# Kernel tuning notes

Measured on AMD Instinct MI355X. Metric: run time of the kernel, lower is better.

## Reference

```python
import jax, jax.numpy as jnp
import numpy as np

N = 100_000   # nodes
E = 600_000   # edges per layer (avg degree ~6, ogbn-arxiv-like)
IN, H, C = 128, 256, 40


def _sage_layer(x, src, dst, w_self, w_neigh, b):
    """DGL SAGEConv with mean aggregator: fc_self(x) + fc_neigh(mean_nbr) + b."""
    n = x.shape[0]
    msg = x[src]                                               # [E, d] gather
    agg = jax.ops.segment_sum(msg, dst, num_segments=n)        # [N, d]
    deg = jax.ops.segment_sum(jnp.ones((src.shape[0],), x.dtype), dst,
                              num_segments=n)                  # [N]
    h_neigh = agg / jnp.maximum(deg, 1.0)[:, None]             # mean; 0 if isolated
    return x @ w_self.T + h_neigh @ w_neigh.T + b


def setup_inputs() -> dict:
    key = jax.random.key(0)
    ks = jax.random.split(key, 11)
    s = 0.02
    return {
        "x": jax.random.normal(ks[0], (N, IN), jnp.float32),
        "src1": jax.random.randint(ks[1], (E,), 0, N, jnp.int32),
        "dst1": jax.random.randint(ks[2], (E,), 0, N, jnp.int32),
        "src2": jax.random.randint(ks[3], (E,), 0, N, jnp.int32),
        "dst2": jax.random.randint(ks[4], (E,), 0, N, jnp.int32),
        "w_self1": s * jax.random.normal(ks[5], (H, IN), jnp.float32),
        "w_neigh1": s * jax.random.normal(ks[6], (H, IN), jnp.float32),
        "b1": jnp.zeros((H,), jnp.float32),
        "w_self2": s * jax.random.normal(ks[7], (C, H), jnp.float32),
        "w_neigh2": s * jax.random.normal(ks[8], (C, H), jnp.float32),
        "b2": jnp.zeros((C,), jnp.float32),
    }


def reference(x, src1, dst1, src2, dst2, w_self1, w_neigh1, b1,
              w_self2, w_neigh2, b2):
    h = jax.nn.relu(_sage_layer(x, src1, dst1, w_self1, w_neigh1, b1))
    return _sage_layer(h, src2, dst2, w_self2, w_neigh2, b2)
```

## Files before the change

### kernel.cpp

```cpp
#include <hip/hip_runtime.h>
#include <hip/hip_bf16.h>
#include <cstdint>
#include <cstddef>


#define D_IN 128
#define D_H  256
#define D_C  40

#define NBLK     128
#define NBKT_MAX 392
#define BKT_CAP  2560

typedef __bf16 bf16_t;
typedef __attribute__((ext_vector_type(8))) __bf16 bf16x8;
typedef __attribute__((ext_vector_type(4))) __bf16 bf16x4;
typedef __attribute__((ext_vector_type(4))) float  f32x4;

static constexpr size_t NMAX = 100000;
static constexpr size_t EMAX = 600000;
static constexpr size_t NSC_MAX = (size_t)NBKT_MAX * NBLK;
static constexpr size_t alignup(size_t v) { return (v + 255) & ~size_t(255); }

static constexpr size_t HG1_OFF  = 0;
static constexpr size_t HG2_OFF  = alignup(HG1_OFF + NSC_MAX * 4);
static constexpr size_t BS1_OFF  = alignup(HG2_OFF + NSC_MAX * 4);
static constexpr size_t BS2_OFF  = alignup(BS1_OFF + 512 * 4);
static constexpr size_t RP1_OFF  = alignup(BS2_OFF + 512 * 4);
static constexpr size_t RP2_OFF  = alignup(RP1_OFF + (NMAX + 1) * 4);
static constexpr size_t BKT1_OFF = alignup(RP2_OFF + (NMAX + 1) * 4);
static constexpr size_t BKT2_OFF = alignup(BKT1_OFF + EMAX * 4);
static constexpr size_t XCAT_OFF = alignup(BKT2_OFF + EMAX * 4);
static constexpr size_t P_OFF    = alignup(XCAT_OFF + (NMAX + 128) * 256 * 2);
static constexpr size_t W1F_OFF  = alignup(P_OFF + NMAX * 40 * 2);
static constexpr size_t W2F_OFF  = alignup(W1F_OFF + 32 * 256 * 8 * 2);
static constexpr size_t WS_NEEDED = W2F_OFF + 32 * 80 * 8 * 2;

__global__ __launch_bounds__(256) void k_prep(
    const float* __restrict__ x, bf16_t* __restrict__ xcat,
    const float* __restrict__ ws1, const float* __restrict__ wn1,
    const float* __restrict__ ws2, const float* __restrict__ wn2,
    bf16_t* __restrict__ w1f, bf16_t* __restrict__ w2f,
    const int* __restrict__ dst1, const int* __restrict__ dst2,
    int* __restrict__ hg1, int* __restrict__ hg2,
    int N, int E, int chunk, int nbkt, int nconvx) {
  __shared__ int h[NBKT_MAX];
  int bid = blockIdx.x;

  if (bid < nconvx) {
    int t = bid * 256 + threadIdx.x;
    if (t < N * 16) {
      int row = t >> 4, j = t & 15;
      const float* sp = x + (size_t)row * 128 + j * 8;
      float4 v0 = ((const float4*)sp)[0];
      float4 v1 = ((const float4*)sp)[1];
      bf16x8 o;
      o[0] = (bf16_t)v0.x; o[1] = (bf16_t)v0.y; o[2] = (bf16_t)v0.z; o[3] = (bf16_t)v0.w;
      o[4] = (bf16_t)v1.x; o[5] = (bf16_t)v1.y; o[6] = (bf16_t)v1.z; o[7] = (bf16_t)v1.w;
      *(bf16x8*)(xcat + (size_t)row * 256 + j * 8) = o;
    }
    return;
  }
  bid -= nconvx;

  if (bid < 32) {
    int t = bid * 256 + threadIdx.x;
    {
      int ks4g = t >> 8, col = t & 255;
      int k0 = (ks4g >> 2) * 32 + (ks4g & 3) * 8;
      bf16x8 o;
#pragma unroll
      for (int i = 0; i < 8; ++i) {
        int k = k0 + i;
        float v = (k < 128) ? ws1[col * 128 + k] : wn1[col * 128 + (k - 128)];
        o[i] = (bf16_t)v;
      }
      *(bf16x8*)(w1f + (size_t)t * 8) = o;
    }
    if (t < 32 * 80) {
      int ks4g = t / 80, col = t - ks4g * 80;
      int k0 = (ks4g >> 2) * 32 + (ks4g & 3) * 8;
      bf16x8 o;
#pragma unroll
      for (int i = 0; i < 8; ++i) {
        int k = k0 + i;
        float v = (col < 40) ? ws2[col * 256 + k] : wn2[(col - 40) * 256 + k];
        o[i] = (bf16_t)v;
      }
      *(bf16x8*)(w2f + (size_t)t * 8) = o;
    }
    return;
  }
  bid -= 32;
  {
    const int* dst = (bid >> 7) ? dst2 : dst1;
    int*       hg  = (bid >> 7) ? hg2 : hg1;
    int        cb  = bid & 127;
    for (int i = threadIdx.x; i < nbkt; i += 256) h[i] = 0;
    __syncthreads();
    int beg = cb * chunk, end = min(E, beg + chunk);
    for (int e = beg + threadIdx.x; e < end; e += 256)
      atomicAdd(&h[dst[e] >> 8], 1);
    __syncthreads();
    for (int b = threadIdx.x; b < nbkt; b += 256)
      hg[b * NBLK + cb] = h[b];
  }
}

__global__ void k_scan_block(int* __restrict__ a1, int* __restrict__ a2,
                             int* __restrict__ b1s, int* __restrict__ b2s, int n) {
  int* a    = blockIdx.y ? a2 : a1;
  int* bsum = blockIdx.y ? b2s : b1s;
  __shared__ int lds[256];
  int t = threadIdx.x, i = blockIdx.x * 256 + t;
  int v = (i < n) ? a[i] : 0;
  lds[t] = v;
  __syncthreads();
  for (int off = 1; off < 256; off <<= 1) {
    int add = (t >= off) ? lds[t - off] : 0;
    __syncthreads();
    lds[t] += add;
    __syncthreads();
  }
  if (i < n) a[i] = lds[t] - v;
  if (t == 255) bsum[blockIdx.x] = lds[255];
}

__global__ void k_scan_addsums(int* __restrict__ a1, int* __restrict__ a2,
                               const int* __restrict__ b1s, const int* __restrict__ b2s,
                               int n, int nb) {
  int* a          = blockIdx.y ? a2 : a1;
  const int* bsum = blockIdx.y ? b2s : b1s;
  __shared__ int lds[256];
  int t = threadIdx.x;
  int v = (t < nb) ? bsum[t] : 0;
  lds[t] = v;
  __syncthreads();
  for (int off = 1; off < 256; off <<= 1) {
    int add = (t >= off) ? lds[t - off] : 0;
    __syncthreads();
    lds[t] += add;
    __syncthreads();
  }
  __shared__ int excl[256];
  excl[t] = lds[t] - v;
  __syncthreads();
  int i = blockIdx.x * 256 + t;
  if (i < n) a[i] += excl[i >> 8];
}

__global__ void k_scat(const int* __restrict__ src1, const int* __restrict__ dst1,
                       const int* __restrict__ src2, const int* __restrict__ dst2,
                       const int* __restrict__ off1, const int* __restrict__ off2,
                       unsigned* __restrict__ bkt1, unsigned* __restrict__ bkt2,
                       int E, int chunk, int nbkt) {
  const int* src = blockIdx.y ? src2 : src1;
  const int* dst = blockIdx.y ? dst2 : dst1;
  const int* off = blockIdx.y ? off2 : off1;
  unsigned*  bkt = blockIdx.y ? bkt2 : bkt1;
  __shared__ int cur[NBKT_MAX];
  for (int i = threadIdx.x; i < nbkt; i += 256)
    cur[i] = off[i * NBLK + blockIdx.x];
  __syncthreads();
  int beg = blockIdx.x * chunk, end = min(E, beg + chunk);
  for (int e = beg + threadIdx.x; e < end; e += 256) {
    int d = dst[e];
    int slot = atomicAdd(&cur[d >> 8], 1);
    bkt[slot] = (unsigned)src[e] | ((unsigned)(d & 255) << 24);
  }
}

__global__ __launch_bounds__(256) void k_bcsr(
    const int* __restrict__ off1, const int* __restrict__ off2,
    const unsigned* bkt1, const unsigned* bkt2,
    int* csr1, int* csr2,
    int* __restrict__ rp1, int* __restrict__ rp2, int E, int N, int nbkt) {
  const int* off      = blockIdx.y ? off2 : off1;
  const unsigned* bkt = blockIdx.y ? bkt2 : bkt1;
  int* csr            = blockIdx.y ? csr2 : csr1;
  int* rowptr         = blockIdx.y ? rp2 : rp1;

  const int b = blockIdx.x, t = threadIdx.x;
  const int base = off[b * NBLK];
  const int endp = (b == nbkt - 1) ? E : off[(b + 1) * NBLK];
  const int cnt  = endp - base;

  __shared__ int hist[256];
  __shared__ int sc[256];
  __shared__ int cur[256];
  __shared__ int stage[BKT_CAP];

  hist[t] = 0;
  __syncthreads();
  for (int i = t; i < cnt; i += 256)
    atomicAdd(&hist[bkt[base + i] >> 24], 1);
  __syncthreads();

  int v = hist[t];
  sc[t] = v;
  __syncthreads();
  for (int off_ = 1; off_ < 256; off_ <<= 1) {
    int add = (t >= off_) ? sc[t - off_] : 0;
    __syncthreads();
    sc[t] += add;
    __syncthreads();
  }
  int excl = sc[t] - v;

  int node = b * 256 + t;
  if (node < N) rowptr[node] = base + excl;
  if (b == nbkt - 1 && t == 0) rowptr[N] = E;
  cur[t] = excl;
  __syncthreads();

  for (int i = t; i < cnt; i += 256) {
    unsigned u = bkt[base + i];
    int slot = atomicAdd(&cur[u >> 24], 1);
    if (slot < BKT_CAP) stage[slot] = (int)(u & 0xFFFFFFu);
  }
  __syncthreads();
  for (int i = t; i < cnt; i += 256)
    csr[base + i] = stage[i];
}

__global__ void k_agg1(bf16_t* __restrict__ xcat, const int* __restrict__ rowptr,
                       const int* __restrict__ csr, int N) {
  int t = blockIdx.x * 256 + threadIdx.x;
  int node = t >> 4, l = t & 15;
  if (node >= N) return;
  int beg = rowptr[node], end = rowptr[node + 1];
  float acc[8] = {0.f, 0.f, 0.f, 0.f, 0.f, 0.f, 0.f, 0.f};
  int e = beg;
  for (; e + 4 <= end; e += 4) {
    int s0 = csr[e], s1 = csr[e + 1], s2 = csr[e + 2], s3 = csr[e + 3];
    bf16x8 v0 = *(const bf16x8*)(xcat + (size_t)s0 * 256 + l * 8);
    bf16x8 v1 = *(const bf16x8*)(xcat + (size_t)s1 * 256 + l * 8);
    bf16x8 v2 = *(const bf16x8*)(xcat + (size_t)s2 * 256 + l * 8);
    bf16x8 v3 = *(const bf16x8*)(xcat + (size_t)s3 * 256 + l * 8);
#pragma unroll
    for (int i = 0; i < 8; ++i)
      acc[i] += (float)v0[i] + (float)v1[i] + (float)v2[i] + (float)v3[i];
  }
  for (; e < end; ++e) {
    int s = csr[e];
    bf16x8 v = *(const bf16x8*)(xcat + (size_t)s * 256 + l * 8);
#pragma unroll
    for (int i = 0; i < 8; ++i) acc[i] += (float)v[i];
  }
  float rd = (end > beg) ? 1.0f / (float)(end - beg) : 0.0f;
  bf16x8 o;
#pragma unroll
  for (int i = 0; i < 8; ++i) o[i] = (bf16_t)(acc[i] * rd);
  *(bf16x8*)(xcat + (size_t)node * 256 + 128 + l * 8) = o;
}

__global__ __launch_bounds__(256, 2) void k_fused(
    const bf16_t* __restrict__ xcat, const bf16_t* __restrict__ w1f,
    const float* __restrict__ b1, const bf16_t* __restrict__ w2f,
    const float* __restrict__ b2v, float* __restrict__ out,
    bf16_t* __restrict__ p, int N) {
  __shared__ __align__(16) char lds[65536];
  const int tid  = (int)threadIdx.x;
  const int wv   = tid >> 6;
  const int lane = tid & 63;
  const int lr   = lane & 15;
  const int lg   = lane >> 4;
  const int c0   = wv * 64;
  const int m0   = (int)blockIdx.x * 128;

  {
    const char* tb = (const char*)(xcat + (size_t)m0 * 256);
#pragma unroll
    for (int i = 0; i < 16; ++i) {
      int L   = i * 4096 + tid * 16;
      int row = L >> 9;
      int c   = L & 511;
      int so  = (row << 9) | (c ^ ((row & 7) << 4));
      __builtin_amdgcn_global_load_lds(
          (const __attribute__((address_space(1))) void*)(tb + so),
          (__attribute__((address_space(3))) void*)(lds + L), 16, 0, 0);
    }
  }
  __syncthreads();

  f32x4 acc[4][8] = {};
#pragma unroll
  for (int ks = 0; ks < 8; ++ks) {
    bf16x8 wf[4];
#pragma unroll
    for (int wb = 0; wb < 4; ++wb)
      wf[wb] = *(const bf16x8*)(w1f + ((size_t)(ks * 4 + lg) * 256 +
                                       (c0 + wb * 16 + lr)) * 8);
    bf16x8 ax[8];
#pragma unroll
    for (int rb = 0; rb < 8; ++rb) {
      int lrow = rb * 16 + lr;
      ax[rb] = *(const bf16x8*)(lds + lrow * 512 +
                                ((ks * 64 + lg * 16) ^ ((lrow & 7) << 4)));
    }
#pragma unroll
    for (int wb = 0; wb < 4; ++wb)
#pragma unroll
      for (int rb = 0; rb < 8; ++rb)
        acc[wb][rb] = __builtin_amdgcn_mfma_f32_16x16x32_bf16(
            wf[wb], ax[rb], acc[wb][rb], 0, 0, 0);
  }

  __syncthreads();

#pragma unroll
  for (int wb = 0; wb < 4; ++wb) {
    float4 b4 = *(const float4*)(b1 + c0 + wb * 16 + lg * 4);
#pragma unroll
    for (int rb = 0; rb < 8; ++rb) {
      int xrow = rb * 16 + lr;
      bf16x4 o;
      o[0] = (bf16_t)fmaxf(acc[wb][rb][0] + b4.x, 0.f);
      o[1] = (bf16_t)fmaxf(acc[wb][rb][1] + b4.y, 0.f);
      o[2] = (bf16_t)fmaxf(acc[wb][rb][2] + b4.z, 0.f);
      o[3] = (bf16_t)fmaxf(acc[wb][rb][3] + b4.w, 0.f);
      *(bf16x4*)(lds + xrow * 512 +
                 ((c0 * 2 + wb * 32 + lg * 8) ^ ((xrow & 7) << 4))) = o;
    }
  }
  __syncthreads();

  f32x4 acc2[2][5] = {};
#pragma unroll
  for (int ks = 0; ks < 8; ++ks) {
    bf16x8 hf[2];
#pragma unroll
    for (int m = 0; m < 2; ++m) {
      int arow = wv * 32 + m * 16 + lr;
      hf[m] = *(const bf16x8*)(lds + arow * 512 +
                               ((ks * 64 + lg * 16) ^ ((arow & 7) << 4)));
    }
#pragma unroll
    for (int wb = 0; wb < 5; ++wb) {
      bf16x8 w2 = *(const bf16x8*)(w2f + ((size_t)(ks * 4 + lg) * 80 +
                                          (wb * 16 + lr)) * 8);
#pragma unroll
      for (int m = 0; m < 2; ++m)
        acc2[m][wb] = __builtin_amdgcn_mfma_f32_16x16x32_bf16(
            w2, hf[m], acc2[m][wb], 0, 0, 0);
    }
  }

#pragma unroll
  for (int m = 0; m < 2; ++m) {
    const int r = m0 + wv * 32 + m * 16 + lr;
    if (r < N) {
#pragma unroll
      for (int wb = 0; wb < 5; ++wb) {
        int col0 = wb * 16 + lg * 4;
        f32x4 v = acc2[m][wb];
        if (col0 < 40) {
          float4 b4 = *(const float4*)(b2v + col0);
          v[0] += b4.x; v[1] += b4.y; v[2] += b4.z; v[3] += b4.w;
          *(f32x4*)(out + (size_t)r * 40 + col0) = v;
        } else {
          bf16x4 o;
          o[0] = (bf16_t)v[0]; o[1] = (bf16_t)v[1];
          o[2] = (bf16_t)v[2]; o[3] = (bf16_t)v[3];
          *(bf16x4*)(p + (size_t)r * 40 + (col0 - 40)) = o;
        }
      }
    }
  }
}

__global__ void k_agg2fin(const bf16_t* __restrict__ p, const int* __restrict__ rowptr,
                          const int* __restrict__ csr, float* __restrict__ out, int N) {
  int t = blockIdx.x * 256 + threadIdx.x;
  int node = t / 10, l = t - node * 10;
  if (node >= N) return;
  int beg = rowptr[node], end = rowptr[node + 1];
  float a0 = 0.f, a1 = 0.f, a2 = 0.f, a3 = 0.f;
  int e = beg;
  for (; e + 4 <= end; e += 4) {
    int s0 = csr[e], s1 = csr[e + 1], s2 = csr[e + 2], s3 = csr[e + 3];
    bf16x4 v0 = *(const bf16x4*)(p + (size_t)s0 * 40 + l * 4);
    bf16x4 v1 = *(const bf16x4*)(p + (size_t)s1 * 40 + l * 4);
    bf16x4 v2 = *(const bf16x4*)(p + (size_t)s2 * 40 + l * 4);
    bf16x4 v3 = *(const bf16x4*)(p + (size_t)s3 * 40 + l * 4);
    a0 += (float)v0[0] + (float)v1[0] + (float)v2[0] + (float)v3[0];
    a1 += (float)v0[1] + (float)v1[1] + (float)v2[1] + (float)v3[1];
    a2 += (float)v0[2] + (float)v1[2] + (float)v2[2] + (float)v3[2];
    a3 += (float)v0[3] + (float)v1[3] + (float)v2[3] + (float)v3[3];
  }
  for (; e < end; ++e) {
    int s = csr[e];
    bf16x4 v = *(const bf16x4*)(p + (size_t)s * 40 + l * 4);
    a0 += (float)v[0]; a1 += (float)v[1]; a2 += (float)v[2]; a3 += (float)v[3];
  }
  float rd = (end > beg) ? 1.0f / (float)(end - beg) : 0.0f;
  float* o = out + (size_t)node * 40 + l * 4;
  float4 cur = *(const float4*)o;
  cur.x += a0 * rd;
  cur.y += a1 * rd;
  cur.z += a2 * rd;
  cur.w += a3 * rd;
  *(float4*)o = cur;
}

extern "C" void kernel_launch(void* const* d_in, const int* in_sizes, int n_in,
                              void* d_out, int out_size, void* d_ws, size_t ws_size,
                              hipStream_t stream) {
  const float* x    = (const float*)d_in[0];
  const int*   src1 = (const int*)d_in[1];
  const int*   dst1 = (const int*)d_in[2];
  const int*   src2 = (const int*)d_in[3];
  const int*   dst2 = (const int*)d_in[4];
  const float* ws1  = (const float*)d_in[5];
  const float* wn1  = (const float*)d_in[6];
  const float* b1   = (const float*)d_in[7];
  const float* ws2  = (const float*)d_in[8];
  const float* wn2  = (const float*)d_in[9];
  const float* b2   = (const float*)d_in[10];
  float*       out  = (float*)d_out;

  const int N = in_sizes[0] / D_IN;
  const int E = in_sizes[1];
  if (ws_size < WS_NEEDED) return;

  char*     ws   = (char*)d_ws;
  int*      hg1  = (int*)(ws + HG1_OFF);
  int*      hg2  = (int*)(ws + HG2_OFF);
  int*      bs1  = (int*)(ws + BS1_OFF);
  int*      bs2  = (int*)(ws + BS2_OFF);
  int*      rp1  = (int*)(ws + RP1_OFF);
  int*      rp2  = (int*)(ws + RP2_OFF);
  unsigned* bkt1 = (unsigned*)(ws + BKT1_OFF);
  unsigned* bkt2 = (unsigned*)(ws + BKT2_OFF);
  int*      csr1 = (int*)(ws + BKT1_OFF);
  int*      csr2 = (int*)(ws + BKT2_OFF);
  bf16_t*   xcat = (bf16_t*)(ws + XCAT_OFF);
  bf16_t*   p    = (bf16_t*)(ws + P_OFF);
  bf16_t*   w1f  = (bf16_t*)(ws + W1F_OFF);
  bf16_t*   w2f  = (bf16_t*)(ws + W2F_OFF);

  const int nbkt  = (N + 255) >> 8;
  const int chunk = (E + NBLK - 1) / NBLK;
  const int nsc   = nbkt * NBLK;
  const int nscb  = (nsc + 255) / 256;
  const int nconvx = (N * 16 + 255) / 256;
  const int ntiles = (N + 127) / 128;

  k_prep<<<nconvx + 32 + 2 * NBLK, 256, 0, stream>>>(
      x, xcat, ws1, wn1, ws2, wn2, w1f, w2f, dst1, dst2, hg1, hg2,
      N, E, chunk, nbkt, nconvx);

  k_scan_block<<<dim3(nscb, 2), 256, 0, stream>>>(hg1, hg2, bs1, bs2, nsc);
  k_scan_addsums<<<dim3(nscb, 2), 256, 0, stream>>>(hg1, hg2, bs1, bs2, nsc, nscb);
  k_scat<<<dim3(NBLK, 2), 256, 0, stream>>>(src1, dst1, src2, dst2, hg1, hg2,
                                            bkt1, bkt2, E, chunk, nbkt);
  k_bcsr<<<dim3(nbkt, 2), 256, 0, stream>>>(hg1, hg2, bkt1, bkt2, csr1, csr2,
                                            rp1, rp2, E, N, nbkt);

  k_agg1<<<(N * 16 + 255) / 256, 256, 0, stream>>>(xcat, rp1, csr1, N);
  k_fused<<<ntiles, 256, 0, stream>>>(xcat, w1f, b1, w2f, b2, out, p, N);
  k_agg2fin<<<(N * 10 + 255) / 256, 256, 0, stream>>>(p, rp2, csr2, out, N);
}
```

Before: 141.8 us.

## Halve fused GEMM tile to 64 rows and software-pipeline fragment loads

Cuts the fused two-layer GEMM tile from 128 to 64 rows, which halves LDS use to 32KB and raises the launch-bounds occupancy hint from 2 to 3 blocks. It also double-buffers the weight and activation fragment loads across the k-steps of both GEMMs so memory latency overlaps with MFMA work. In exchange, each weight fragment is now reused over fewer rows, so total weight traffic doubles and twice as many blocks are launched.

```diff
diff --git a/kernel.cpp b/kernel.cpp
--- a/kernel.cpp
+++ b/kernel.cpp
@@ -254,24 +254,24 @@
   *(bf16x8*)(xcat + (size_t)node * 256 + 128 + l * 8) = o;
 }
 
-__global__ __launch_bounds__(256, 2) void k_fused(
+__global__ __launch_bounds__(256, 3) void k_fused(
     const bf16_t* __restrict__ xcat, const bf16_t* __restrict__ w1f,
     const float* __restrict__ b1, const bf16_t* __restrict__ w2f,
     const float* __restrict__ b2v, float* __restrict__ out,
     bf16_t* __restrict__ p, int N) {
-  __shared__ __align__(16) char lds[65536];
+  __shared__ __align__(16) char lds[32768];
   const int tid  = (int)threadIdx.x;
   const int wv   = tid >> 6;
   const int lane = tid & 63;
   const int lr   = lane & 15;
   const int lg   = lane >> 4;
   const int c0   = wv * 64;
-  const int m0   = (int)blockIdx.x * 128;
+  const int m0   = (int)blockIdx.x * 64;
 
   {
     const char* tb = (const char*)(xcat + (size_t)m0 * 256);
 #pragma unroll
-    for (int i = 0; i < 16; ++i) {
+    for (int i = 0; i < 8; ++i) {
       int L   = i * 4096 + tid * 16;
       int row = L >> 9;
       int c   = L & 511;
@@ -281,29 +281,48 @@
           (__attribute__((address_space(3))) void*)(lds + L), 16, 0, 0);
     }
   }
-  __syncthreads();
-
-  f32x4 acc[4][8] = {};
+
+  bf16x8 wfc[4];
+#pragma unroll
+  for (int wb = 0; wb < 4; ++wb)
+    wfc[wb] = *(const bf16x8*)(w1f + ((size_t)(0 * 4 + lg) * 256 +
+                                      (c0 + wb * 16 + lr)) * 8);
+  __syncthreads();
+
+  bf16x8 axc[4];
+#pragma unroll
+  for (int rb = 0; rb < 4; ++rb) {
+    int lrow = rb * 16 + lr;
+    axc[rb] = *(const bf16x8*)(lds + lrow * 512 +
+                               ((0 * 64 + lg * 16) ^ ((lrow & 7) << 4)));
+  }
+
+  f32x4 acc[4][4] = {};
 #pragma unroll
   for (int ks = 0; ks < 8; ++ks) {
-    bf16x8 wf[4];
+    bf16x8 wfn[4], axn[4];
+    if (ks < 7) {
+#pragma unroll
+      for (int wb = 0; wb < 4; ++wb)
+        wfn[wb] = *(const bf16x8*)(w1f + ((size_t)((ks + 1) * 4 + lg) * 256 +
+                                          (c0 + wb * 16 + lr)) * 8);
+#pragma unroll
+      for (int rb = 0; rb < 4; ++rb) {
+        int lrow = rb * 16 + lr;
+        axn[rb] = *(const bf16x8*)(lds + lrow * 512 +
+                                   (((ks + 1) * 64 + lg * 16) ^ ((lrow & 7) << 4)));
+      }
+    }
 #pragma unroll
     for (int wb = 0; wb < 4; ++wb)
-      wf[wb] = *(const bf16x8*)(w1f + ((size_t)(ks * 4 + lg) * 256 +
-                                       (c0 + wb * 16 + lr)) * 8);
-    bf16x8 ax[8];
-#pragma unroll
-    for (int rb = 0; rb < 8; ++rb) {
-      int lrow = rb * 16 + lr;
-      ax[rb] = *(const bf16x8*)(lds + lrow * 512 +
-                                ((ks * 64 + lg * 16) ^ ((lrow & 7) << 4)));
-    }
-#pragma unroll
-    for (int wb = 0; wb < 4; ++wb)
-#pragma unroll
-      for (int rb = 0; rb < 8; ++rb)
+#pragma unroll
+      for (int rb = 0; rb < 4; ++rb)
         acc[wb][rb] = __builtin_amdgcn_mfma_f32_16x16x32_bf16(
-            wf[wb], ax[rb], acc[wb][rb], 0, 0, 0);
+            wfc[wb], axc[rb], acc[wb][rb], 0, 0, 0);
+    if (ks < 7) {
+#pragma unroll
+      for (int i = 0; i < 4; ++i) { wfc[i] = wfn[i]; axc[i] = axn[i]; }
+    }
   }
 
   __syncthreads();
@@ -312,7 +331,7 @@
   for (int wb = 0; wb < 4; ++wb) {
     float4 b4 = *(const float4*)(b1 + c0 + wb * 16 + lg * 4);
 #pragma unroll
-    for (int rb = 0; rb < 8; ++rb) {
+    for (int rb = 0; rb < 4; ++rb) {
       int xrow = rb * 16 + lr;
       bf16x4 o;
       o[0] = (bf16_t)fmaxf(acc[wb][rb][0] + b4.x, 0.f);
@@ -325,45 +344,53 @@
   }
   __syncthreads();
 
-  f32x4 acc2[2][5] = {};
+  const int arow = wv * 16 + lr;
+  bf16x8 hfc = *(const bf16x8*)(lds + arow * 512 +
+                                ((0 * 64 + lg * 16) ^ ((arow & 7) << 4)));
+  bf16x8 w2c[5];
+#pragma unroll
+  for (int wb = 0; wb < 5; ++wb)
+    w2c[wb] = *(const bf16x8*)(w2f + ((size_t)(0 * 4 + lg) * 80 +
+                                      (wb * 16 + lr)) * 8);
+
+  f32x4 acc2[5] = {};
 #pragma unroll
   for (int ks = 0; ks < 8; ++ks) {
-    bf16x8 hf[2];
-#pragma unroll
-    for (int m = 0; m < 2; ++m) {
-      int arow = wv * 32 + m * 16 + lr;
-      hf[m] = *(const bf16x8*)(lds + arow * 512 +
-                               ((ks * 64 + lg * 16) ^ ((arow & 7) << 4)));
-    }
+    bf16x8 hfn, w2n[5];
+    if (ks < 7) {
+      hfn = *(const bf16x8*)(lds + arow * 512 +
+                             (((ks + 1) * 64 + lg * 16) ^ ((arow & 7) << 4)));
+#pragma unroll
+      for (int wb = 0; wb < 5; ++wb)
+        w2n[wb] = *(const bf16x8*)(w2f + ((size_t)((ks + 1) * 4 + lg) * 80 +
+                                          (wb * 16 + lr)) * 8);
+    }
+#pragma unroll
+    for (int wb = 0; wb < 5; ++wb)
+      acc2[wb] = __builtin_amdgcn_mfma_f32_16x16x32_bf16(
+          w2c[wb], hfc, acc2[wb], 0, 0, 0);
+    if (ks < 7) {
+      hfc = hfn;
+#pragma unroll
+      for (int i = 0; i < 5; ++i) w2c[i] = w2n[i];
+    }
+  }
+
+  const int r = m0 + wv * 16 + lr;
+  if (r < N) {
 #pragma unroll
     for (int wb = 0; wb < 5; ++wb) {
-      bf16x8 w2 = *(const bf16x8*)(w2f + ((size_t)(ks * 4 + lg) * 80 +
-                                          (wb * 16 + lr)) * 8);
-#pragma unroll
-      for (int m = 0; m < 2; ++m)
-        acc2[m][wb] = __builtin_amdgcn_mfma_f32_16x16x32_bf16(
-            w2, hf[m], acc2[m][wb], 0, 0, 0);
-    }
-  }
-
-#pragma unroll
-  for (int m = 0; m < 2; ++m) {
-    const int r = m0 + wv * 32 + m * 16 + lr;
-    if (r < N) {
-#pragma unroll
-      for (int wb = 0; wb < 5; ++wb) {
-        int col0 = wb * 16 + lg * 4;
-        f32x4 v = acc2[m][wb];
-        if (col0 < 40) {
-          float4 b4 = *(const float4*)(b2v + col0);
-          v[0] += b4.x; v[1] += b4.y; v[2] += b4.z; v[3] += b4.w;
-          *(f32x4*)(out + (size_t)r * 40 + col0) = v;
-        } else {
-          bf16x4 o;
-          o[0] = (bf16_t)v[0]; o[1] = (bf16_t)v[1];
-          o[2] = (bf16_t)v[2]; o[3] = (bf16_t)v[3];
-          *(bf16x4*)(p + (size_t)r * 40 + (col0 - 40)) = o;
-        }
+      int col0 = wb * 16 + lg * 4;
+      f32x4 v = acc2[wb];
+      if (col0 < 40) {
+        float4 b4 = *(const float4*)(b2v + col0);
+        v[0] += b4.x; v[1] += b4.y; v[2] += b4.z; v[3] += b4.w;
+        *(f32x4*)(out + (size_t)r * 40 + col0) = v;
+      } else {
+        bf16x4 o;
+        o[0] = (bf16_t)v[0]; o[1] = (bf16_t)v[1];
+        o[2] = (bf16_t)v[2]; o[3] = (bf16_t)v[3];
+        *(bf16x4*)(p + (size_t)r * 40 + (col0 - 40)) = o;
       }
     }
   }
@@ -444,7 +471,7 @@
   const int nsc   = nbkt * NBLK;
   const int nscb  = (nsc + 255) / 256;
   const int nconvx = (N * 16 + 255) / 256;
-  const int ntiles = (N + 127) / 128;
+  const int ntiles = (N + 63) / 64;
 
   k_prep<<<nconvx + 32 + 2 * NBLK, 256, 0, stream>>>(
       x, xcat, ws1, wn1, ws2, wn2, w1f, w2f, dst1, dst2, hg1, hg2,
```

After: 136.5 us. 1.04x faster.

## Stage W1 in LDS and stream activation rows directly per wave in fused kernel

Applied to the files above, without the earlier changes.

Restructures the fused two-layer GEMM kernel. It now uses 512 threads and 256-row tiles, stages the whole 128KB layer-1 weight matrix in LDS, and has each wave read its own 32 activation rows straight from global memory. Each wave computes all 256 hidden columns for its rows and writes the ReLU output to a private LDS region, so the block-wide barrier before layer 2 becomes a local waitcnt. The weight layout in the prep kernel is reordered to match. The cost is 128KB of LDS per block, which limits occupancy, and global-latency-bound loads of the activation rows.

```diff
diff --git a/kernel.cpp b/kernel.cpp
--- a/kernel.cpp
+++ b/kernel.cpp
@@ -31,9 +31,9 @@
 static constexpr size_t BKT1_OFF = alignup(RP2_OFF + (NMAX + 1) * 4);
 static constexpr size_t BKT2_OFF = alignup(BKT1_OFF + EMAX * 4);
 static constexpr size_t XCAT_OFF = alignup(BKT2_OFF + EMAX * 4);
-static constexpr size_t P_OFF    = alignup(XCAT_OFF + (NMAX + 128) * 256 * 2);
+static constexpr size_t P_OFF    = alignup(XCAT_OFF + (NMAX + 256) * 256 * 2);
 static constexpr size_t W1F_OFF  = alignup(P_OFF + NMAX * 40 * 2);
-static constexpr size_t W2F_OFF  = alignup(W1F_OFF + 32 * 256 * 8 * 2);
+static constexpr size_t W2F_OFF  = alignup(W1F_OFF + 8192 * 16);
 static constexpr size_t WS_NEEDED = W2F_OFF + 32 * 80 * 8 * 2;
 
 __global__ __launch_bounds__(256) void k_prep(
@@ -66,8 +66,9 @@
   if (bid < 32) {
     int t = bid * 256 + threadIdx.x;
     {
-      int ks4g = t >> 8, col = t & 255;
-      int k0 = (ks4g >> 2) * 32 + (ks4g & 3) * 8;
+      int lr = t & 15, lg = (t >> 4) & 3, wb = (t >> 6) & 15, ks = t >> 10;
+      int col = wb * 16 + lr;
+      int k0  = ks * 32 + lg * 8;
       bf16x8 o;
 #pragma unroll
       for (int i = 0; i < 8; ++i) {
@@ -254,76 +255,66 @@
   *(bf16x8*)(xcat + (size_t)node * 256 + 128 + l * 8) = o;
 }
 
-__global__ __launch_bounds__(256, 2) void k_fused(
+__global__ __launch_bounds__(512, 2) void k_fused(
     const bf16_t* __restrict__ xcat, const bf16_t* __restrict__ w1f,
     const float* __restrict__ b1, const bf16_t* __restrict__ w2f,
     const float* __restrict__ b2v, float* __restrict__ out,
     bf16_t* __restrict__ p, int N) {
-  __shared__ __align__(16) char lds[65536];
-  const int tid  = (int)threadIdx.x;
-  const int wv   = tid >> 6;
-  const int lane = tid & 63;
-  const int lr   = lane & 15;
-  const int lg   = lane >> 4;
-  const int c0   = wv * 64;
-  const int m0   = (int)blockIdx.x * 128;
-
-  {
-    const char* tb = (const char*)(xcat + (size_t)m0 * 256);
-#pragma unroll
-    for (int i = 0; i < 16; ++i) {
-      int L   = i * 4096 + tid * 16;
-      int row = L >> 9;
-      int c   = L & 511;
-      int so  = (row << 9) | (c ^ ((row & 7) << 4));
-      __builtin_amdgcn_global_load_lds(
-          (const __attribute__((address_space(1))) void*)(tb + so),
-          (__attribute__((address_space(3))) void*)(lds + L), 16, 0, 0);
-    }
-  }
-  __syncthreads();
-
-  f32x4 acc[4][8] = {};
+  __shared__ __align__(16) char lds[131072];
+  const int tid   = (int)threadIdx.x;
+  const int wv    = tid >> 6;
+  const int lane  = tid & 63;
+  const int lr    = lane & 15;
+  const int lg    = lane >> 4;
+  const int m0    = (int)blockIdx.x * 256;
+  const int rbase = m0 + wv * 32;
+
+#pragma unroll
+  for (int i = 0; i < 16; ++i) {
+    int off = (i * 512 + tid) * 16;
+    __builtin_amdgcn_global_load_lds(
+        (const __attribute__((address_space(1))) void*)((const char*)w1f + off),
+        (__attribute__((address_space(3))) void*)(lds + off), 16, 0, 0);
+  }
+
+  int r0i = rbase + lr, r1i = rbase + 16 + lr;
+  const bf16_t* xr0 = xcat + (size_t)(r0i < N ? r0i : N - 1) * 256 + lg * 8;
+  const bf16_t* xr1 = xcat + (size_t)(r1i < N ? r1i : N - 1) * 256 + lg * 8;
+
+  __syncthreads();
+
+  f32x4 acc[16][2] = {};
 #pragma unroll
   for (int ks = 0; ks < 8; ++ks) {
-    bf16x8 wf[4];
-#pragma unroll
-    for (int wb = 0; wb < 4; ++wb)
-      wf[wb] = *(const bf16x8*)(w1f + ((size_t)(ks * 4 + lg) * 256 +
-                                       (c0 + wb * 16 + lr)) * 8);
-    bf16x8 ax[8];
-#pragma unroll
-    for (int rb = 0; rb < 8; ++rb) {
+    bf16x8 ax0 = *(const bf16x8*)(xr0 + ks * 32);
+    bf16x8 ax1 = *(const bf16x8*)(xr1 + ks * 32);
+#pragma unroll
+    for (int wb = 0; wb < 16; ++wb) {
+      bf16x8 wf = *(const bf16x8*)(lds + ((((ks * 16 + wb) * 4 + lg) * 16 + lr) << 4));
+      acc[wb][0] = __builtin_amdgcn_mfma_f32_16x16x32_bf16(wf, ax0, acc[wb][0], 0, 0, 0);
+      acc[wb][1] = __builtin_amdgcn_mfma_f32_16x16x32_bf16(wf, ax1, acc[wb][1], 0, 0, 0);
+    }
+  }
+
+  __syncthreads();
+
+  char* hb = lds + wv * 16384;
+#pragma unroll
+  for (int wb = 0; wb < 16; ++wb) {
+    float4 b4 = *(const float4*)(b1 + wb * 16 + lg * 4);
+#pragma unroll
+    for (int rb = 0; rb < 2; ++rb) {
       int lrow = rb * 16 + lr;
-      ax[rb] = *(const bf16x8*)(lds + lrow * 512 +
-                                ((ks * 64 + lg * 16) ^ ((lrow & 7) << 4)));
-    }
-#pragma unroll
-    for (int wb = 0; wb < 4; ++wb)
-#pragma unroll
-      for (int rb = 0; rb < 8; ++rb)
-        acc[wb][rb] = __builtin_amdgcn_mfma_f32_16x16x32_bf16(
-            wf[wb], ax[rb], acc[wb][rb], 0, 0, 0);
-  }
-
-  __syncthreads();
-
-#pragma unroll
-  for (int wb = 0; wb < 4; ++wb) {
-    float4 b4 = *(const float4*)(b1 + c0 + wb * 16 + lg * 4);
-#pragma unroll
-    for (int rb = 0; rb < 8; ++rb) {
-      int xrow = rb * 16 + lr;
       bf16x4 o;
       o[0] = (bf16_t)fmaxf(acc[wb][rb][0] + b4.x, 0.f);
       o[1] = (bf16_t)fmaxf(acc[wb][rb][1] + b4.y, 0.f);
       o[2] = (bf16_t)fmaxf(acc[wb][rb][2] + b4.z, 0.f);
       o[3] = (bf16_t)fmaxf(acc[wb][rb][3] + b4.w, 0.f);
-      *(bf16x4*)(lds + xrow * 512 +
-                 ((c0 * 2 + wb * 32 + lg * 8) ^ ((xrow & 7) << 4))) = o;
-    }
-  }
-  __syncthreads();
+      *(bf16x4*)(hb + lrow * 512 + ((wb * 32 + lg * 8) ^ ((lrow & 7) << 4))) = o;
+    }
+  }
+  asm volatile("s_waitcnt lgkmcnt(0)" ::: "memory");
+  __builtin_amdgcn_sched_barrier(0);
 
   f32x4 acc2[2][5] = {};
 #pragma unroll
@@ -331,9 +322,8 @@
     bf16x8 hf[2];
 #pragma unroll
     for (int m = 0; m < 2; ++m) {
-      int arow = wv * 32 + m * 16 + lr;
-      hf[m] = *(const bf16x8*)(lds + arow * 512 +
-                               ((ks * 64 + lg * 16) ^ ((arow & 7) << 4)));
+      int ar = m * 16 + lr;
+      hf[m] = *(const bf16x8*)(hb + ar * 512 + ((ks * 64 + lg * 16) ^ ((ar & 7) << 4)));
     }
 #pragma unroll
     for (int wb = 0; wb < 5; ++wb) {
@@ -348,7 +338,7 @@
 
 #pragma unroll
   for (int m = 0; m < 2; ++m) {
-    const int r = m0 + wv * 32 + m * 16 + lr;
+    const int r = rbase + m * 16 + lr;
     if (r < N) {
 #pragma unroll
       for (int wb = 0; wb < 5; ++wb) {
@@ -444,7 +434,7 @@
   const int nsc   = nbkt * NBLK;
   const int nscb  = (nsc + 255) / 256;
   const int nconvx = (N * 16 + 255) / 256;
-  const int ntiles = (N + 127) / 128;
+  const int ntiles = (N + 255) / 256;
 
   k_prep<<<nconvx + 32 + 2 * NBLK, 256, 0, stream>>>(
       x, xcat, ws1, wn1, ws2, wn2, w1f, w2f, dst1, dst2, hg1, hg2,
@@ -458,6 +448,6 @@
                                             rp1, rp2, E, N, nbkt);
 
   k_agg1<<<(N * 16 + 255) / 256, 256, 0, stream>>>(xcat, rp1, csr1, N);
-  k_fused<<<ntiles, 256, 0, stream>>>(xcat, w1f, b1, w2f, b2, out, p, N);
+  k_fused<<<ntiles, 512, 0, stream>>>(xcat, w1f, b1, w2f, b2, out, p, N);
   k_agg2fin<<<(N * 10 + 255) / 256, 256, 0, stream>>>(p, rp2, csr2, out, N);
 }
```

Measured after the change: 136.9 us. 1.04x faster.
